# Kernel tuning notes

Measured on AMD Instinct MI355X. Metric: run time of the kernel, lower is better.

## Reference

```python
import jax, jax.numpy as jnp
import numpy as np

C, I, O = 32, 1024, 1024
B, T = 64, 512


def setup_inputs() -> dict:
    key = jax.random.key(0)
    kx, kc, kw, kb = jax.random.split(key, 4)
    x = jax.random.normal(kx, (B, T, I), dtype=jnp.float32)
    cat_ids = jax.random.randint(kc, (B,), 0, C)
    W = 0.02 * jax.random.normal(kw, (C, I, O), dtype=jnp.float32)
    b = jnp.zeros((C, O), dtype=jnp.float32)
    return {"x": x, "cat_ids": cat_ids, "W": W, "b": b}


def reference(x, cat_ids, W, b):
    # Per-category affine: y[b] = x[b] @ W[cat_ids[b]] + b[cat_ids[b]]
    selected_W = W[cat_ids]            # [B, I, O] (gathered per batch element)
    selected_b = b[cat_ids]            # [B, O]
    if x.ndim == 2:
        return jnp.einsum('bi,bio->bo', x, selected_W) + selected_b
    return jnp.einsum('bti,bio->bto', x, selected_W) + selected_b[:, None, :]
```

## Files before the change

### kernel.cpp

```cpp
#include <hip/hip_runtime.h>
#include <stdint.h>

#define CATS  32
#define DI    1024
#define DO    1024
#define NB    64
#define ST    512

#define BM 128
#define BN 128
#define BK 32
#define NSTEP (DI / BK)

typedef float  f32x4  __attribute__((ext_vector_type(4)));
typedef short  bf16x8 __attribute__((ext_vector_type(8)));

__device__ __forceinline__ uint32_t cvt_pk_bf16(float lo, float hi) {
    uint32_t r;
    asm("v_cvt_pk_bf16_f32 %0, %1, %2" : "=v"(r) : "v"(lo), "v"(hi));
    return r;
}

struct Regs {
    f32x4 ra[4];
    f32x4 rb0[2], rb1[2];
};

__global__ __launch_bounds__(256, 2) void fused_cat_gemm_kernel(
        const float* __restrict__ x, const int* __restrict__ cat_ids,
        const float* __restrict__ W, const float* __restrict__ bias,
        float* __restrict__ out) {
    __shared__ __align__(16) unsigned short As[2][BM * BK];
    __shared__ __align__(16) unsigned short Bs[2][BN * BK];

    const int fb = blockIdx.x;
    const int vv = (fb & 7) * 256 + (fb >> 3);
    const int b     = vv >> 5;
    const int mbase = ((vv >> 3) & 3) * BM;
    const int nbase = (vv & 7) * BN;
    const int cat   = cat_ids[b];

    const int tid  = threadIdx.x;
    const int lane = tid & 63;
    const int w    = tid >> 6;
    const int wr   = w >> 1;
    const int wc   = w & 1;
    const int l15  = lane & 15;
    const int kg   = lane >> 4;
    const int koff = (kg ^ ((l15 >> 1) & 3)) * 8;

    const int am   = tid >> 3;
    const int ak   = (tid & 7) * 4;
    const int ac   = (ak >> 3) ^ ((am >> 1) & 3);
    const int aoff = am * BK + ac * 8 + (ak & 4);
    const float* gA = x + (size_t)(b * ST + mbase + am) * DI + ak;

    const int bq  = tid >> 3;
    const int bk2 = lane & 7;
    const float* gB = W + (size_t)cat * DI * DO + nbase + bq * 4;

    f32x4 acc[4][4];
    #pragma unroll
    for (int mi = 0; mi < 4; ++mi)
        #pragma unroll
        for (int ni = 0; ni < 4; ++ni)
            acc[mi][ni] = (f32x4){0.f, 0.f, 0.f, 0.f};

    auto LOADS = [&](Regs& R, int step) {
        #pragma unroll
        for (int q = 0; q < 4; ++q)
            R.ra[q] = *(const f32x4*)(gA + (size_t)q * 32 * DI + step * BK);
        #pragma unroll
        for (int u = 0; u < 2; ++u) {
            const float* p = gB + (size_t)(step * BK + (bk2 + 8 * u) * 2) * DO;
            R.rb0[u] = *(const f32x4*)p;
            R.rb1[u] = *(const f32x4*)(p + DO);
        }
    };

    auto WRITES = [&](int bufi, Regs& R) {
        #pragma unroll
        for (int q = 0; q < 4; ++q) {
            uint2 pk;
            pk.x = cvt_pk_bf16(R.ra[q][0], R.ra[q][1]);
            pk.y = cvt_pk_bf16(R.ra[q][2], R.ra[q][3]);
            *(uint2*)&As[bufi][aoff + q * 32 * BK] = pk;
        }
        #pragma unroll
        for (int u = 0; u < 2; ++u) {
            const int k2 = bk2 + 8 * u;
            #pragma unroll
            for (int j = 0; j < 4; ++j) {
                const int n = bq * 4 + j;
                const int c = ((k2 >> 2) ^ (n >> 1)) & 3;
                *(uint32_t*)&Bs[bufi][n * BK + c * 8 + (k2 & 3) * 2] =
                    cvt_pk_bf16(R.rb0[u][j], R.rb1[u][j]);
            }
        }
    };

    auto MFMA_STEP = [&](int bufc) {
        bf16x8 af[4], bfr[4];
        #pragma unroll
        for (int mi = 0; mi < 4; ++mi)
            af[mi] = *(const bf16x8*)&As[bufc][(wr * 64 + mi * 16 + l15) * BK + koff];
        #pragma unroll
        for (int ni = 0; ni < 4; ++ni)
            bfr[ni] = *(const bf16x8*)&Bs[bufc][(wc * 64 + ni * 16 + l15) * BK + koff];
        #pragma unroll
        for (int mi = 0; mi < 4; ++mi)
            #pragma unroll
            for (int ni = 0; ni < 4; ++ni)
                acc[mi][ni] = __builtin_amdgcn_mfma_f32_16x16x32_bf16(
                                  af[mi], bfr[ni], acc[mi][ni], 0, 0, 0);
    };

    #define LGKM_BARRIER()                                      \
        do {                                                    \
            asm volatile("s_waitcnt lgkmcnt(0)" ::: "memory");  \
            __builtin_amdgcn_s_barrier();                       \
        } while (0)

    Regs r0, r1;
    LOADS(r0, 0);
    WRITES(0, r0);
    LOADS(r1, 1);
    LGKM_BARRIER();

    #pragma unroll 1
    for (int s = 0; s < NSTEP; s += 2) {
        if (s + 2 < NSTEP) LOADS(r0, s + 2);
        MFMA_STEP(0);
        WRITES(1, r1);
        LGKM_BARRIER();

        if (s + 3 < NSTEP) LOADS(r1, s + 3);
        MFMA_STEP(1);
        if (s + 2 < NSTEP) WRITES(0, r0);
        LGKM_BARRIER();
    }
    #undef LGKM_BARRIER

    float bsv[4];
    #pragma unroll
    for (int ni = 0; ni < 4; ++ni)
        bsv[ni] = bias[(size_t)cat * DO + nbase + wc * 64 + ni * 16 + l15];

    #pragma unroll
    for (int mi = 0; mi < 4; ++mi) {
        const int rowb = mbase + wr * 64 + mi * 16 + kg * 4;
        #pragma unroll
        for (int r = 0; r < 4; ++r) {
            float* orow = out + (size_t)(b * ST + rowb + r) * DO
                              + nbase + wc * 64 + l15;
            #pragma unroll
            for (int ni = 0; ni < 4; ++ni)
                orow[ni * 16] = acc[mi][ni][r] + bsv[ni];
        }
    }
}

extern "C" void kernel_launch(void* const* d_in, const int* in_sizes, int n_in,
                              void* d_out, int out_size, void* d_ws, size_t ws_size,
                              hipStream_t stream) {
    const float* x    = (const float*)d_in[0];
    const int*   cats = (const int*)d_in[1];
    const float* W    = (const float*)d_in[2];
    const float* bias = (const float*)d_in[3];
    float*       out  = (float*)d_out;

    (void)d_ws; (void)ws_size;

    fused_cat_gemm_kernel<<<NB * (ST / BM) * (DO / BN), 256, 0, stream>>>(
        x, cats, W, bias, out);
}
```

Baseline: 428.0 us.

## Enlarge GEMM tiles to 256x128x64 with 512-thread blocks and XOR-swizzled LDS

Doubles the M tile and K step and moves to 8 waves per block, so each block reuses more of the gathered W tile and each x tile across more MFMAs. Global loads are rewritten as wider per-thread row chunks, stored to LDS as 16-byte packed bf16 with an 8-way XOR swizzle. The main loop interleaves next-step loads and LDS writes between two half-K MFMA groups, with s_setprio raised around the MFMAs. In exchange, LDS use grows to about 96KB per block, which likely limits occupancy to one block per CU, and register prefetch is now only one step deep.

```diff
diff --git a/kernel.cpp b/kernel.cpp
--- a/kernel.cpp
+++ b/kernel.cpp
@@ -7,12 +7,14 @@
 #define NB    64
 #define ST    512
 
-#define BM 128
+#define BM 256
 #define BN 128
-#define BK 32
+#define BK 64
 #define NSTEP (DI / BK)
+#define NBLK  (NB * (ST / BM) * (DO / BN))
 
 typedef float  f32x4  __attribute__((ext_vector_type(4)));
+typedef float  f32x2  __attribute__((ext_vector_type(2)));
 typedef short  bf16x8 __attribute__((ext_vector_type(8)));
 
 __device__ __forceinline__ uint32_t cvt_pk_bf16(float lo, float hi) {
@@ -21,12 +23,7 @@
     return r;
 }
 
-struct Regs {
-    f32x4 ra[4];
-    f32x4 rb0[2], rb1[2];
-};
-
-__global__ __launch_bounds__(256, 2) void fused_cat_gemm_kernel(
+__global__ __launch_bounds__(512, 2) void fused_cat_gemm_kernel(
         const float* __restrict__ x, const int* __restrict__ cat_ids,
         const float* __restrict__ W, const float* __restrict__ bias,
         float* __restrict__ out) {
@@ -34,9 +31,9 @@
     __shared__ __align__(16) unsigned short Bs[2][BN * BK];
 
     const int fb = blockIdx.x;
-    const int vv = (fb & 7) * 256 + (fb >> 3);
-    const int b     = vv >> 5;
-    const int mbase = ((vv >> 3) & 3) * BM;
+    const int vv = (fb & 7) * 128 + (fb >> 3);
+    const int b     = vv >> 4;
+    const int mbase = ((vv >> 3) & 1) * BM;
     const int nbase = (vv & 7) * BN;
     const int cat   = cat_ids[b];
 
@@ -47,17 +44,35 @@
     const int wc   = w & 1;
     const int l15  = lane & 15;
     const int kg   = lane >> 4;
-    const int koff = (kg ^ ((l15 >> 1) & 3)) * 8;
-
-    const int am   = tid >> 3;
-    const int ak   = (tid & 7) * 4;
-    const int ac   = (ak >> 3) ^ ((am >> 1) & 3);
-    const int aoff = am * BK + ac * 8 + (ak & 4);
-    const float* gA = x + (size_t)(b * ST + mbase + am) * DI + ak;
-
-    const int bq  = tid >> 3;
-    const int bk2 = lane & 7;
-    const float* gB = W + (size_t)cat * DI * DO + nbase + bq * 4;
+
+    const int arow = tid >> 1;
+    const int ah   = tid & 1;
+    const int axr  = (arow & 7) ^ ((arow >> 3) & 7);
+    const float* gA = x + (size_t)(b * ST + mbase + arow) * DI + ah * 32;
+
+    const int np  = tid & 63;
+    const int kc8 = tid >> 6;
+    int bxr[2];
+    #pragma unroll
+    for (int j = 0; j < 2; ++j) {
+        const int nr = np * 2 + j;
+        bxr[j] = (nr & 7) ^ ((nr >> 3) & 7);
+    }
+    const float* gB = W + ((size_t)cat * DI + kc8 * 8) * DO + nbase + np * 2;
+
+    int offA[4], offB[4];
+    #pragma unroll
+    for (int mi = 0; mi < 4; ++mi) {
+        const int row = wr * 64 + mi * 16 + l15;
+        const int rx  = (l15 & 7) ^ ((2 * mi + (l15 >> 3)) & 7);
+        offA[mi] = row * BK + ((kg ^ rx) * 8);
+    }
+    #pragma unroll
+    for (int ni = 0; ni < 4; ++ni) {
+        const int row = wc * 64 + ni * 16 + l15;
+        const int rx  = (l15 & 7) ^ ((2 * ni + (l15 >> 3)) & 7);
+        offB[ni] = row * BK + ((kg ^ rx) * 8);
+    }
 
     f32x4 acc[4][4];
     #pragma unroll
@@ -66,53 +81,60 @@
         for (int ni = 0; ni < 4; ++ni)
             acc[mi][ni] = (f32x4){0.f, 0.f, 0.f, 0.f};
 
-    auto LOADS = [&](Regs& R, int step) {
-        #pragma unroll
-        for (int q = 0; q < 4; ++q)
-            R.ra[q] = *(const f32x4*)(gA + (size_t)q * 32 * DI + step * BK);
-        #pragma unroll
-        for (int u = 0; u < 2; ++u) {
-            const float* p = gB + (size_t)(step * BK + (bk2 + 8 * u) * 2) * DO;
-            R.rb0[u] = *(const f32x4*)p;
-            R.rb1[u] = *(const f32x4*)(p + DO);
+    f32x4 ra[8];
+    f32x2 rb[8];
+
+    auto LOADS_A = [&](int s) {
+        #pragma unroll
+        for (int q = 0; q < 8; ++q)
+            ra[q] = *(const f32x4*)(gA + (size_t)s * BK + q * 4);
+    };
+    auto LOADS_B = [&](int s) {
+        #pragma unroll
+        for (int q = 0; q < 8; ++q)
+            rb[q] = *(const f32x2*)(gB + (size_t)(s * BK + q) * DO);
+    };
+    auto WRITES_A = [&](int bufi) {
+        #pragma unroll
+        for (int j = 0; j < 4; ++j) {
+            const int c = (ah * 4 + j) ^ axr;
+            uint4 pk;
+            pk.x = cvt_pk_bf16(ra[2 * j][0], ra[2 * j][1]);
+            pk.y = cvt_pk_bf16(ra[2 * j][2], ra[2 * j][3]);
+            pk.z = cvt_pk_bf16(ra[2 * j + 1][0], ra[2 * j + 1][1]);
+            pk.w = cvt_pk_bf16(ra[2 * j + 1][2], ra[2 * j + 1][3]);
+            *(uint4*)&As[bufi][arow * BK + c * 8] = pk;
         }
     };
-
-    auto WRITES = [&](int bufi, Regs& R) {
-        #pragma unroll
-        for (int q = 0; q < 4; ++q) {
-            uint2 pk;
-            pk.x = cvt_pk_bf16(R.ra[q][0], R.ra[q][1]);
-            pk.y = cvt_pk_bf16(R.ra[q][2], R.ra[q][3]);
-            *(uint2*)&As[bufi][aoff + q * 32 * BK] = pk;
+    auto WRITES_B = [&](int bufi) {
+        #pragma unroll
+        for (int j = 0; j < 2; ++j) {
+            const int nrow = np * 2 + j;
+            const int c    = kc8 ^ bxr[j];
+            uint4 pk;
+            pk.x = cvt_pk_bf16(rb[0][j], rb[1][j]);
+            pk.y = cvt_pk_bf16(rb[2][j], rb[3][j]);
+            pk.z = cvt_pk_bf16(rb[4][j], rb[5][j]);
+            pk.w = cvt_pk_bf16(rb[6][j], rb[7][j]);
+            *(uint4*)&Bs[bufi][nrow * BK + c * 8] = pk;
         }
-        #pragma unroll
-        for (int u = 0; u < 2; ++u) {
-            const int k2 = bk2 + 8 * u;
-            #pragma unroll
-            for (int j = 0; j < 4; ++j) {
-                const int n = bq * 4 + j;
-                const int c = ((k2 >> 2) ^ (n >> 1)) & 3;
-                *(uint32_t*)&Bs[bufi][n * BK + c * 8 + (k2 & 3) * 2] =
-                    cvt_pk_bf16(R.rb0[u][j], R.rb1[u][j]);
-            }
-        }
-    };
-
-    auto MFMA_STEP = [&](int bufc) {
-        bf16x8 af[4], bfr[4];
+    };
+    auto COMPUTE = [&](int bufc, int kk) {
+        bf16x8 af[4], bfv[4];
+        #pragma unroll
+        for (int ni = 0; ni < 4; ++ni)
+            bfv[ni] = *(const bf16x8*)&Bs[bufc][offB[ni] ^ (kk * 32)];
         #pragma unroll
         for (int mi = 0; mi < 4; ++mi)
-            af[mi] = *(const bf16x8*)&As[bufc][(wr * 64 + mi * 16 + l15) * BK + koff];
-        #pragma unroll
-        for (int ni = 0; ni < 4; ++ni)
-            bfr[ni] = *(const bf16x8*)&Bs[bufc][(wc * 64 + ni * 16 + l15) * BK + koff];
+            af[mi] = *(const bf16x8*)&As[bufc][offA[mi] ^ (kk * 32)];
+        __builtin_amdgcn_s_setprio(1);
         #pragma unroll
         for (int mi = 0; mi < 4; ++mi)
             #pragma unroll
             for (int ni = 0; ni < 4; ++ni)
                 acc[mi][ni] = __builtin_amdgcn_mfma_f32_16x16x32_bf16(
-                                  af[mi], bfr[ni], acc[mi][ni], 0, 0, 0);
+                                  af[mi], bfv[ni], acc[mi][ni], 0, 0, 0);
+        __builtin_amdgcn_s_setprio(0);
     };
 
     #define LGKM_BARRIER()                                      \
@@ -121,23 +143,26 @@
             __builtin_amdgcn_s_barrier();                       \
         } while (0)
 
-    Regs r0, r1;
-    LOADS(r0, 0);
-    WRITES(0, r0);
-    LOADS(r1, 1);
+    LOADS_A(0);
+    LOADS_B(0);
+    WRITES_A(0);
+    WRITES_B(0);
     LGKM_BARRIER();
+
+    auto STEP = [&](int s, int bufc, bool pre) {
+        if (pre) LOADS_A(s + 1);
+        COMPUTE(bufc, 0);
+        if (pre) LOADS_B(s + 1);
+        if (pre) WRITES_A(bufc ^ 1);
+        COMPUTE(bufc, 1);
+        if (pre) WRITES_B(bufc ^ 1);
+        LGKM_BARRIER();
+    };
 
     #pragma unroll 1
     for (int s = 0; s < NSTEP; s += 2) {
-        if (s + 2 < NSTEP) LOADS(r0, s + 2);
-        MFMA_STEP(0);
-        WRITES(1, r1);
-        LGKM_BARRIER();
-
-        if (s + 3 < NSTEP) LOADS(r1, s + 3);
-        MFMA_STEP(1);
-        if (s + 2 < NSTEP) WRITES(0, r0);
-        LGKM_BARRIER();
+        STEP(s, 0, true);
+        STEP(s + 1, 1, s + 2 < NSTEP);
     }
     #undef LGKM_BARRIER
 
@@ -171,6 +196,5 @@
 
     (void)d_ws; (void)ws_size;
 
-    fused_cat_gemm_kernel<<<NB * (ST / BM) * (DO / BN), 256, 0, stream>>>(
-        x, cats, W, bias, out);
+    fused_cat_gemm_kernel<<<NBLK, 512, 0, stream>>>(x, cats, W, bias, out);
 }
```

After: 461.4 us. 1.08x slower.
